# Kernel tuning notes

Hardware: AMD Instinct MI355X
Metric: run time of the kernel (lower is better)

Reference implementation:

```python
import jax, jax.numpy as jnp
import numpy as np
from jax import lax

MASK_STEEP = 4.0
MASK_SHIFT = 0.5
RESIST_TH = 0.225
RESIST_STEEP = 50.0
MAX_DOSE = 1.02
MIN_DOSE = 0.98
KD = 35  # kernel_dim1 == kernel_dim2


def setup_inputs() -> dict:
    key = jax.random.key(0)
    ks = jax.random.split(key, 7)
    N, H, W, K = 2, 1024, 1024, 24
    return {
        "mask_tile": jax.random.uniform(ks[0], (N, 1, H, W), dtype=jnp.float32),
        "kernel_focus_r": jax.random.normal(ks[1], (K, KD, KD), dtype=jnp.float32) * 0.02,
        "kernel_focus_i": jax.random.normal(ks[2], (K, KD, KD), dtype=jnp.float32) * 0.02,
        "kernel_defocus_r": jax.random.normal(ks[3], (K, KD, KD), dtype=jnp.float32) * 0.02,
        "kernel_defocus_i": jax.random.normal(ks[4], (K, KD, KD), dtype=jnp.float32) * 0.02,
        "kernel_focus_scale": jax.random.uniform(ks[5], (K, 1, 1), dtype=jnp.float32),
        "kernel_defocus_scale": jax.random.uniform(ks[6], (K, 1, 1), dtype=jnp.float32),
    }


def _avepool3(x):
    # nn.AvgPool2d(kernel=3, stride=1, pad=1) with count_include_pad=True ==
    # conv with a 3x3 ones/9 kernel and zero padding.
    k = jnp.ones((1, 1, 3, 3), x.dtype) / 9.0
    return lax.conv_general_dilated(
        x, k, window_strides=(1, 1), padding=[(1, 1), (1, 1)],
        dimension_numbers=("NCHW", "OIHW", "NCHW"))


def _dose_branch(spec, dose, kernel, scale, h, w):
    # spec: [N,1,KD,KD] complex; kernel: [K,KD,KD] complex; scale: [K,1,1]
    x = (spec * dose) * kernel[None]                 # [N,K,KD,KD] (repeat_interleave via broadcast, C=1)
    x = jnp.fft.ifft2(x, s=(h, w))                   # zero-pad to full tile, [N,K,h,w] complex
    inten = (x.real * x.real + x.imag * x.imag) * scale[None]
    inten = jnp.sum(inten, axis=1, keepdims=True)    # [N,1,h,w]
    resist = jax.nn.sigmoid(RESIST_STEEP * (inten - RESIST_TH))
    return resist, inten


def reference(mask_tile, kernel_focus_r, kernel_focus_i, kernel_defocus_r,
              kernel_defocus_i, kernel_focus_scale, kernel_defocus_scale):
    n, _, h, w = mask_tile.shape
    off = h // 2 - KD // 2
    mask = _avepool3(mask_tile)
    mask = jax.nn.sigmoid(MASK_STEEP * (mask - MASK_SHIFT))
    mf = jnp.fft.fftshift(jnp.fft.fft2(mask), axes=(-2, -1))  # [N,1,h,w] complex64
    spec = mf[:, :, off:off + KD, off:off + KD]               # [N,1,KD,KD]
    kf = kernel_focus_r + 1j * kernel_focus_i
    kdf = kernel_defocus_r + 1j * kernel_defocus_i
    nominal, x_out = _dose_branch(spec, 1.0, kf, kernel_focus_scale, h, w)
    outer, x_out_max = _dose_branch(spec, MAX_DOSE, kf, kernel_focus_scale, h, w)
    inner, x_out_min = _dose_branch(spec, MIN_DOSE, kdf, kernel_defocus_scale, h, w)
    return (nominal, inner, outer, x_out, x_out_min, x_out_max)
```

## Files before the change

kernel.cpp:

```cpp
#include <hip/hip_runtime.h>
#include <math.h>

#define NBATCH 2
#define HH 1024
#define WW 1024
#define KKER 24
#define KDIM 35
#define NPIX (HH*WW)
#define KSQ (KDIM*KDIM)
#define NDA 69
#define NTAU 9
#define NFR 18
#define VCOLS 43

#define G_OFF 0
#define S_OFF (G_OFF + NBATCH*HH*NFR*2)
#define VP_OFF (S_OFF + NBATCH*KSQ*2)
#define V_OFF (VP_OFF + NBATCH*2*KKER*NDA*KDIM*2)

__device__ __forceinline__ float2 cmadd(float2 p, float2 w, float2 u) {
    return make_float2(fmaf(p.x, w.x, fmaf(-p.y, w.y, u.x)),
                       fmaf(p.x, w.y, fmaf( p.y, w.x, u.y)));
}
__device__ __forceinline__ float sigm(float v) {
    return 1.f / (1.f + expf(-v));
}

__global__ __launch_bounds__(320) void fwd_rows(const float* __restrict__ mt, float* __restrict__ ws) {
    __shared__ __align__(16) float vs[1024];
    __shared__ float row[1056];
    __shared__ float2 twl[1024];
    __shared__ float2 P[16 * NFR];
    int bid = blockIdx.x;
    int n = bid >> 10, y = bid & 1023;
    int t = threadIdx.x;
    const float* base = mt + (size_t)n * NPIX;
    if (t < 256) {
        float4 a = ((const float4*)(base + (size_t)y * WW))[t];
        if (y > 0)    { float4 b = ((const float4*)(base + (size_t)(y - 1) * WW))[t];
                        a.x += b.x; a.y += b.y; a.z += b.z; a.w += b.w; }
        if (y < 1023) { float4 b = ((const float4*)(base + (size_t)(y + 1) * WW))[t];
                        a.x += b.x; a.y += b.y; a.z += b.z; a.w += b.w; }
        ((float4*)vs)[t] = a;
    }
    for (int j = t; j < 1024; j += 320) {
        float s, c;
        sincospif(-2.0f * (float)j * (1.0f / 1024.0f), &s, &c);
        twl[j] = make_float2(c, s);
    }
    __syncthreads();
    for (int x = t; x < 1024; x += 320) {
        float s = vs[x];
        if (x > 0)    s += vs[x - 1];
        if (x < 1023) s += vs[x + 1];
        s *= (1.0f / 9.0f);
        row[x + (x >> 5)] = sigm(4.0f * (s - 0.5f));
    }
    __syncthreads();
    if (t < 16 * NFR) {
        int q = t / NFR, m = t - q * NFR;
        float2 cm = twl[m];
        float ar = 0.f, ai = 0.f;
        #pragma unroll
        for (int sc = 0; sc < 2; ++sc) {
            int xs = q * 64 + sc * 32;
            unsigned j0 = ((unsigned)(m * xs)) & 1023u;
            float2 wv = twl[j0];
            float wr = wv.x, wi = wv.y;
            int rb = xs + (xs >> 5);
            #pragma unroll
            for (int i = 0; i < 32; ++i) {
                float val = row[rb + i];
                ar = fmaf(val, wr, ar);
                ai = fmaf(val, wi, ai);
                float nwr = fmaf(wr, cm.x, -wi * cm.y);
                float nwi = fmaf(wr, cm.y,  wi * cm.x);
                wr = nwr; wi = nwi;
            }
        }
        P[t] = make_float2(ar, ai);
    }
    __syncthreads();
    if (t < NFR) {
        float gr = 0.f, gi = 0.f;
        #pragma unroll
        for (int q = 0; q < 16; ++q) {
            gr += P[q * NFR + t].x;
            gi += P[q * NFR + t].y;
        }
        float2* Gp = (float2*)(ws + G_OFF) + (size_t)(n * HH + y) * NFR + t;
        *Gp = make_float2(gr, gi);
    }
}

__global__ __launch_bounds__(1024) void fwd_cols(float* __restrict__ ws) {
    __shared__ float2 twl[1024];
    __shared__ float2 P[56 * NFR];
    int bid = blockIdx.x;
    int t = threadIdx.x;
    int n = bid / KDIM, a = bid - n * KDIM;
    {
        float s, c;
        sincospif(-2.0f * (float)t * (1.0f / 1024.0f), &s, &c);
        twl[t] = make_float2(c, s);
    }
    __syncthreads();
    if (t < 56 * NFR) {
        int g = t / NFR, mb = t - NFR * g;
        int ys = (g << 10) / 56, ye = ((g + 1) << 10) / 56;
        int ma = a - 17;
        const float2* Gp = (const float2*)(ws + G_OFF) + (size_t)n * HH * NFR + mb;
        float ar = 0.f, ai = 0.f;
        for (int y = ys; y < ye; ++y) {
            float2 g2 = Gp[(size_t)y * NFR];
            float2 cc = twl[((unsigned)(ma * y)) & 1023u];
            ar = fmaf(g2.x, cc.x, ar); ar = fmaf(-g2.y, cc.y, ar);
            ai = fmaf(g2.x, cc.y, ai); ai = fmaf( g2.y, cc.x, ai);
        }
        P[t] = make_float2(ar, ai);
    }
    __syncthreads();
    if (t < NFR) {
        float sr = 0.f, si = 0.f;
        #pragma unroll
        for (int g = 0; g < 56; ++g) { sr += P[g * NFR + t].x; si += P[g * NFR + t].y; }
        float2* Sp = (float2*)(ws + S_OFF) + (size_t)n * KSQ;
        Sp[a * KDIM + (17 + t)] = make_float2(sr, si);
        if (t > 0)
            Sp[(34 - a) * KDIM + (17 - t)] = make_float2(sr, -si);
    }
}

__global__ __launch_bounds__(512) void mk_V(float* __restrict__ ws,
        const float* __restrict__ kfr, const float* __restrict__ kfi,
        const float* __restrict__ kdr, const float* __restrict__ kdi,
        const float* __restrict__ kfs, const float* __restrict__ kds) {
    __shared__ float2 Xp[KDIM * VCOLS];
    __shared__ float2 Vp[9][8][8];
    int bid = blockIdx.x;
    int tau = bid % NTAU; int r = bid / NTAU;
    int k = r % KKER; r /= KKER;
    int br = r & 1; int n = r >> 1;
    int t = threadIdx.x;
    for (int i = t; i < KDIM * VCOLS; i += 512) Xp[i] = make_float2(0.f, 0.f);
    __syncthreads();
    const float* kr = (br ? kdr : kfr) + (size_t)k * KSQ;
    const float* ki = (br ? kdi : kfi) + (size_t)k * KSQ;
    const float* sp = ws + S_OFF + (size_t)n * KSQ * 2;
    for (int i = t; i < KSQ; i += 512) {
        int a = i / KDIM, b = i - a * KDIM;
        float srr = sp[2*i], sii = sp[2*i + 1];
        float krr = kr[i], kii = ki[i];
        Xp[a * VCOLS + b] = make_float2(srr * krr - sii * kii, srr * kii + sii * krr);
    }
    __syncthreads();

    int wv = t >> 6, lane = t & 63;
    int apSlot = lane & 7, dai8 = lane >> 3;
    int dai = tau * 8 + dai8, da = dai - 34;
    int daiHi = tau * 8 + 7; if (daiHi > NDA - 1) daiHi = NDA - 1;
    int apLo = -(daiHi - 34); if (apLo < 0) apLo = 0;
    int apHi = KDIM - (tau * 8 - 34); if (apHi > KDIM) apHi = KDIM;
    bool lv = (dai < NDA);

    int oct = (wv < 3) ? 0 : (wv < 5) ? 1 : (wv < 7) ? 2 : 3;
    int b0w = (wv == 1) ? 12 : (wv == 2) ? 24 : (wv == 4) ? 13 : (wv == 6) ? 9 : 0;
    int b1w = (wv == 0) ? 12 : (wv == 1) ? 24 : (wv == 2) ? 35 :
              (wv == 3) ? 13 : (wv == 4) ? 27 : (wv == 5) ? 9  :
              (wv == 6) ? 19 : 11;
    int npass = (wv == 7) ? 2 : 1;
    for (int p = 0; p < npass; ++p) {
        int db0 = p ? 32 : oct * 8;
        int b0  = p ? 0  : b0w;
        int b1  = p ? 3  : b1w;
        int slot = p ? 8 : wv;
        float2 acc[8];
        #pragma unroll
        for (int j = 0; j < 8; ++j) acc[j] = make_float2(0.f, 0.f);
        for (int ap = apLo + apSlot; ap < apHi; ap += 8) {
            if (lv && ((unsigned)(ap + da) < (unsigned)KDIM)) {
                const float2* rx = Xp + (ap + da) * VCOLS + db0;
                const float2* ry = Xp + ap * VCOLS;
                float2 w[8];
                #pragma unroll
                for (int j = 0; j < 8; ++j) w[j] = rx[b0 + j];
                int bp = b0;
                for (; bp + 8 <= b1; bp += 8) {
                    #pragma unroll
                    for (int u = 0; u < 8; ++u) {
                        float2 yv = ry[bp + u];
                        #pragma unroll
                        for (int j = 0; j < 8; ++j) {
                            acc[j].x = fmaf(w[j].x, yv.x, acc[j].x);
                            acc[j].x = fmaf(w[j].y, yv.y, acc[j].x);
                            acc[j].y = fmaf(w[j].y, yv.x, acc[j].y);
                            acc[j].y = fmaf(-w[j].x, yv.y, acc[j].y);
                        }
                        #pragma unroll
                        for (int j = 0; j < 7; ++j) w[j] = w[j + 1];
                        w[7] = rx[bp + u + 8];
                    }
                }
                for (; bp < b1; ++bp) {
                    float2 yv = ry[bp];
                    #pragma unroll
                    for (int j = 0; j < 8; ++j) {
                        acc[j].x = fmaf(w[j].x, yv.x, acc[j].x);
                        acc[j].x = fmaf(w[j].y, yv.y, acc[j].x);
                        acc[j].y = fmaf(w[j].y, yv.x, acc[j].y);
                        acc[j].y = fmaf(-w[j].x, yv.y, acc[j].y);
                    }
                    #pragma unroll
                    for (int j = 0; j < 7; ++j) w[j] = w[j + 1];
                    w[7] = rx[bp + 8];
                }
            }
        }
        #pragma unroll
        for (int j = 0; j < 8; ++j) {
            acc[j].x += __shfl_xor(acc[j].x, 1); acc[j].y += __shfl_xor(acc[j].y, 1);
            acc[j].x += __shfl_xor(acc[j].x, 2); acc[j].y += __shfl_xor(acc[j].y, 2);
            acc[j].x += __shfl_xor(acc[j].x, 4); acc[j].y += __shfl_xor(acc[j].y, 4);
        }
        if (apSlot == 0) {
            #pragma unroll
            for (int j = 0; j < 8; ++j) Vp[slot][dai8][j] = acc[j];
        }
    }
    __syncthreads();
    if (t < 8 * KDIM) {
        int d8 = t / KDIM, db = t - d8 * KDIM;
        int dai2 = tau * 8 + d8;
        if (dai2 < NDA) {
            int oc = db >> 3, j = db & 7;
            float2 sum;
            if (oc == 0) {
                sum = make_float2(Vp[0][d8][j].x + Vp[1][d8][j].x + Vp[2][d8][j].x,
                                  Vp[0][d8][j].y + Vp[1][d8][j].y + Vp[2][d8][j].y);
            } else if (oc == 1) {
                sum = make_float2(Vp[3][d8][j].x + Vp[4][d8][j].x,
                                  Vp[3][d8][j].y + Vp[4][d8][j].y);
            } else if (oc == 2) {
                sum = make_float2(Vp[5][d8][j].x + Vp[6][d8][j].x,
                                  Vp[5][d8][j].y + Vp[6][d8][j].y);
            } else if (oc == 3) {
                sum = Vp[7][d8][j];
            } else {
                sum = Vp[8][d8][j];
            }
            float s = (br ? kds[k] * (0.98f * 0.98f) : kfs[k]) * 0x1p-40f;
            int nb = n * 2 + br;
            ((float2*)(ws + VP_OFF))[(((size_t)nb * KKER + k) * NDA + dai2) * KDIM + db] =
                make_float2(s * sum.x, s * sum.y);
        }
    }
}

__global__ __launch_bounds__(64) void reduce_V(float* __restrict__ ws) {
    int bid = blockIdx.x;
    int nb = bid / NDA, dai = bid - nb * NDA;
    int t = threadIdx.x;
    if (t < KDIM) {
        const float2* vp = (const float2*)(ws + VP_OFF);
        float sr = 0.f, si = 0.f;
        #pragma unroll
        for (int k = 0; k < KKER; ++k) {
            float2 v = vp[(((size_t)nb * KKER + k) * NDA + dai) * KDIM + t];
            sr += v.x; si += v.y;
        }
        ((float2*)(ws + V_OFF))[((size_t)nb * NDA + dai) * KDIM + t] = make_float2(sr, si);
    }
}

#define YPB 2
__global__ __launch_bounds__(256) void litho_fused(const float* __restrict__ ws,
                                                   float* __restrict__ out) {
    __shared__ float2 twl[1024];
    __shared__ float2 Vl[NDA * KDIM];
    __shared__ float2 Ul[YPB][KDIM];
    int bid = blockIdx.x;
    int yc = bid & 511; int nb = bid >> 9;
    int t = threadIdx.x;
    for (int j = t; j < 1024; j += 256) {
        float s, c;
        sincospif(-2.0f * (float)j * (1.0f / 1024.0f), &s, &c);
        twl[j] = make_float2(c, s);
    }
    const float2* Vg = (const float2*)(ws + V_OFF) + (size_t)nb * NDA * KDIM;
    for (int i = t; i < NDA * KDIM; i += 256) Vl[i] = Vg[i];
    __syncthreads();
    if (t < YPB * KDIM) {
        int yl = t / KDIM, db = t - yl * KDIM;
        int y = yc * YPB + yl;
        float ar = 0.f, ai = 0.f;
        for (int dai = 0; dai < NDA; ++dai) {
            float2 cc = twl[((unsigned)(y * (dai - 34))) & 1023u];
            float cr = cc.x, ci = -cc.y;
            float2 v = Vl[dai * KDIM + db];
            ar = fmaf(v.x, cr, ar); ar = fmaf(-v.y, ci, ar);
            ai = fmaf(v.x, ci, ai); ai = fmaf( v.y, cr, ai);
        }
        Ul[yl][db] = make_float2(ar, ai);
    }
    __syncthreads();
    int n = nb >> 1, br = nb & 1;
    float2 z  = twl[t];              z.y  = -z.y;
    float2 z2 = twl[(2*t) & 1023];   z2.y = -z2.y;
    float2 z3 = twl[(3*t) & 1023];   z3.y = -z3.y;
    float2 w  = twl[(4*t) & 1023];   w.y  = -w.y;
    const size_t OS = (size_t)NBATCH * NPIX;
    #pragma unroll
    for (int yl = 0; yl < YPB; ++yl) {
        int y = yc * YPB + yl;
        float2 P0 = Ul[yl][32], P1 = Ul[yl][33], P2 = Ul[yl][34], P3 = make_float2(0.f, 0.f);
        #pragma unroll
        for (int q = 7; q >= 0; --q) {
            P0 = cmadd(P0, w, Ul[yl][4*q]);
            P1 = cmadd(P1, w, Ul[yl][4*q+1]);
            P2 = cmadd(P2, w, Ul[yl][4*q+2]);
            P3 = cmadd(P3, w, Ul[yl][4*q+3]);
        }
        float U0r = Ul[yl][0].x;
        float A1x = P1.x * z.x  - P1.y * z.y,  A1y = P1.x * z.y  + P1.y * z.x;
        float A2x = P2.x * z2.x - P2.y * z2.y;
        float A3x = P3.x * z3.x - P3.y * z3.y, A3y = P3.x * z3.y + P3.y * z3.x;
        float Re4[4];
        Re4[0] = P0.x + A1x + A2x + A3x;
        Re4[1] = P0.x - A1y - A2x + A3y;
        Re4[2] = P0.x - A1x + A2x - A3x;
        Re4[3] = P0.x + A1y - A2x - A3y;
        size_t obase = (size_t)n * NPIX + (size_t)y * WW;
        if (br == 0) {
            #pragma unroll
            for (int c = 0; c < 4; ++c) {
                int x = t + c * 256;
                float If   = fmaf(2.f, Re4[c], -U0r);
                float Imax = If * (1.02f * 1.02f);
                out[0 * OS + obase + x] = sigm(50.f * (If   - 0.225f));
                out[2 * OS + obase + x] = sigm(50.f * (Imax - 0.225f));
                out[3 * OS + obase + x] = If;
                out[5 * OS + obase + x] = Imax;
            }
        } else {
            #pragma unroll
            for (int c = 0; c < 4; ++c) {
                int x = t + c * 256;
                float Id = fmaf(2.f, Re4[c], -U0r);
                out[1 * OS + obase + x] = sigm(50.f * (Id - 0.225f));
                out[4 * OS + obase + x] = Id;
            }
        }
    }
}

extern "C" void kernel_launch(void* const* d_in, const int* in_sizes, int n_in,
                              void* d_out, int out_size, void* d_ws, size_t ws_size,
                              hipStream_t stream) {
    (void)in_sizes; (void)n_in; (void)out_size; (void)ws_size;
    const float* mt  = (const float*)d_in[0];
    const float* kfr = (const float*)d_in[1];
    const float* kfi = (const float*)d_in[2];
    const float* kdr = (const float*)d_in[3];
    const float* kdi = (const float*)d_in[4];
    const float* kfs = (const float*)d_in[5];
    const float* kds = (const float*)d_in[6];
    float* out = (float*)d_out;
    float* ws  = (float*)d_ws;

    hipLaunchKernelGGL(fwd_rows,    dim3(NBATCH * HH),              dim3(320),  0, stream, mt, ws);
    hipLaunchKernelGGL(fwd_cols,    dim3(NBATCH * KDIM),            dim3(1024), 0, stream, ws);
    hipLaunchKernelGGL(mk_V,        dim3(NBATCH * 2 * KKER * NTAU), dim3(512),  0, stream,
                       ws, kfr, kfi, kdr, kdi, kfs, kds);
    hipLaunchKernelGGL(reduce_V,    dim3(NBATCH * 2 * NDA),         dim3(64),   0, stream, ws);
    hipLaunchKernelGGL(litho_fused, dim3(NBATCH * 2 * 512),         dim3(256),  0, stream, ws, out);
}
```

Before: 154.9 us.

## Fuse column DFT, V build, reduce and output into one persistent kernel

New measurement: 369.7 us. 139% more time.

```diff
diff --git a/kernel.cpp b/kernel.cpp
--- a/kernel.cpp
+++ b/kernel.cpp
@@ -12,11 +12,15 @@
 #define NTAU 9
 #define NFR 18
 #define VCOLS 43
+#define NVBLK (NBATCH*2*KKER*NTAU)
+#define GRID2 1024
+#define COLS_BASE (GRID2 - NBATCH*KDIM)
 
 #define G_OFF 0
 #define S_OFF (G_OFF + NBATCH*HH*NFR*2)
 #define VP_OFF (S_OFF + NBATCH*KSQ*2)
 #define V_OFF (VP_OFF + NBATCH*2*KKER*NDA*KDIM*2)
+#define CNT_OFF (V_OFF + NBATCH*2*NDA*KDIM*2)
 
 __device__ __forceinline__ float2 cmadd(float2 p, float2 w, float2 u) {
     return make_float2(fmaf(p.x, w.x, fmaf(-p.y, w.y, u.x)),
@@ -24,6 +28,13 @@
 }
 __device__ __forceinline__ float sigm(float v) {
     return 1.f / (1.f + expf(-v));
+}
+__device__ __forceinline__ void wait_cnt(int* p, int target) {
+    if (threadIdx.x == 0) {
+        while (atomicAdd(p, 0) < target) __builtin_amdgcn_s_sleep(16);
+    }
+    __syncthreads();
+    __threadfence();
 }
 
 __global__ __launch_bounds__(320) void fwd_rows(const float* __restrict__ mt, float* __restrict__ ws) {
@@ -34,6 +45,7 @@
     int bid = blockIdx.x;
     int n = bid >> 10, y = bid & 1023;
     int t = threadIdx.x;
+    if (bid == 0 && t < 8) ((int*)(ws + CNT_OFF))[t] = 0;
     const float* base = mt + (size_t)n * NPIX;
     if (t < 256) {
         float4 a = ((const float4*)(base + (size_t)y * WW))[t];
@@ -93,102 +105,137 @@
     }
 }
 
-__global__ __launch_bounds__(1024) void fwd_cols(float* __restrict__ ws) {
-    __shared__ float2 twl[1024];
-    __shared__ float2 P[56 * NFR];
-    int bid = blockIdx.x;
-    int t = threadIdx.x;
-    int n = bid / KDIM, a = bid - n * KDIM;
-    {
-        float s, c;
-        sincospif(-2.0f * (float)t * (1.0f / 1024.0f), &s, &c);
-        twl[t] = make_float2(c, s);
-    }
-    __syncthreads();
-    if (t < 56 * NFR) {
-        int g = t / NFR, mb = t - NFR * g;
-        int ys = (g << 10) / 56, ye = ((g + 1) << 10) / 56;
-        int ma = a - 17;
-        const float2* Gp = (const float2*)(ws + G_OFF) + (size_t)n * HH * NFR + mb;
-        float ar = 0.f, ai = 0.f;
-        for (int y = ys; y < ye; ++y) {
-            float2 g2 = Gp[(size_t)y * NFR];
-            float2 cc = twl[((unsigned)(ma * y)) & 1023u];
-            ar = fmaf(g2.x, cc.x, ar); ar = fmaf(-g2.y, cc.y, ar);
-            ai = fmaf(g2.x, cc.y, ai); ai = fmaf( g2.y, cc.x, ai);
-        }
-        P[t] = make_float2(ar, ai);
-    }
-    __syncthreads();
-    if (t < NFR) {
-        float sr = 0.f, si = 0.f;
-        #pragma unroll
-        for (int g = 0; g < 56; ++g) { sr += P[g * NFR + t].x; si += P[g * NFR + t].y; }
-        float2* Sp = (float2*)(ws + S_OFF) + (size_t)n * KSQ;
-        Sp[a * KDIM + (17 + t)] = make_float2(sr, si);
-        if (t > 0)
-            Sp[(34 - a) * KDIM + (17 - t)] = make_float2(sr, -si);
-    }
-}
-
-__global__ __launch_bounds__(512) void mk_V(float* __restrict__ ws,
+__global__ __launch_bounds__(256, 5) void mega2(
         const float* __restrict__ kfr, const float* __restrict__ kfi,
         const float* __restrict__ kdr, const float* __restrict__ kdi,
-        const float* __restrict__ kfs, const float* __restrict__ kds) {
-    __shared__ float2 Xp[KDIM * VCOLS];
-    __shared__ float2 Vp[9][8][8];
-    int bid = blockIdx.x;
-    int tau = bid % NTAU; int r = bid / NTAU;
-    int k = r % KKER; r /= KKER;
-    int br = r & 1; int n = r >> 1;
-    int t = threadIdx.x;
-    for (int i = t; i < KDIM * VCOLS; i += 512) Xp[i] = make_float2(0.f, 0.f);
-    __syncthreads();
-    const float* kr = (br ? kdr : kfr) + (size_t)k * KSQ;
-    const float* ki = (br ? kdi : kfi) + (size_t)k * KSQ;
-    const float* sp = ws + S_OFF + (size_t)n * KSQ * 2;
-    for (int i = t; i < KSQ; i += 512) {
-        int a = i / KDIM, b = i - a * KDIM;
-        float srr = sp[2*i], sii = sp[2*i + 1];
-        float krr = kr[i], kii = ki[i];
-        Xp[a * VCOLS + b] = make_float2(srr * krr - sii * kii, srr * kii + sii * krr);
-    }
-    __syncthreads();
-
-    int wv = t >> 6, lane = t & 63;
-    int apSlot = lane & 7, dai8 = lane >> 3;
-    int dai = tau * 8 + dai8, da = dai - 34;
-    int daiHi = tau * 8 + 7; if (daiHi > NDA - 1) daiHi = NDA - 1;
-    int apLo = -(daiHi - 34); if (apLo < 0) apLo = 0;
-    int apHi = KDIM - (tau * 8 - 34); if (apHi > KDIM) apHi = KDIM;
-    bool lv = (dai < NDA);
-
-    int oct = (wv < 3) ? 0 : (wv < 5) ? 1 : (wv < 7) ? 2 : 3;
-    int b0w = (wv == 1) ? 12 : (wv == 2) ? 24 : (wv == 4) ? 13 : (wv == 6) ? 9 : 0;
-    int b1w = (wv == 0) ? 12 : (wv == 1) ? 24 : (wv == 2) ? 35 :
-              (wv == 3) ? 13 : (wv == 4) ? 27 : (wv == 5) ? 9  :
-              (wv == 6) ? 19 : 11;
-    int npass = (wv == 7) ? 2 : 1;
-    for (int p = 0; p < npass; ++p) {
-        int db0 = p ? 32 : oct * 8;
-        int b0  = p ? 0  : b0w;
-        int b1  = p ? 3  : b1w;
-        int slot = p ? 8 : wv;
-        float2 acc[8];
+        const float* __restrict__ kfs, const float* __restrict__ kds,
+        float* __restrict__ out, float* __restrict__ ws) {
+    __shared__ float2 twl[1024];
+    __shared__ union {
+        struct { float2 P[14 * NFR]; } A;
+        struct { float2 Xp[KDIM * VCOLS]; float2 Vp[9][8][8]; } B;
+        struct { float2 Vl[NDA * KDIM]; float2 Ul[4][KDIM]; } C;
+    } sm;
+    __shared__ int winner;
+    int bid = blockIdx.x, t = threadIdx.x;
+    int* cnt = (int*)(ws + CNT_OFF);
+
+    for (int j = t; j < 1024; j += 256) {
+        float s, c;
+        sincospif(-2.0f * (float)j * (1.0f / 1024.0f), &s, &c);
+        twl[j] = make_float2(c, s);
+    }
+    __syncthreads();
+
+    if (bid >= COLS_BASE) {
+        int cbid = bid - COLS_BASE;
+        int n = cbid / KDIM, a = cbid - n * KDIM;
+        if (t < 14 * NFR) {
+            int g = t / NFR, mb = t - NFR * g;
+            int ys = (g << 10) / 14, ye = ((g + 1) << 10) / 14;
+            int ma = a - 17;
+            const float2* Gp = (const float2*)(ws + G_OFF) + (size_t)n * HH * NFR + mb;
+            float ar = 0.f, ai = 0.f;
+            for (int y = ys; y < ye; ++y) {
+                float2 g2 = Gp[(size_t)y * NFR];
+                float2 cc = twl[((unsigned)(ma * y)) & 1023u];
+                ar = fmaf(g2.x, cc.x, ar); ar = fmaf(-g2.y, cc.y, ar);
+                ai = fmaf(g2.x, cc.y, ai); ai = fmaf( g2.y, cc.x, ai);
+            }
+            sm.A.P[t] = make_float2(ar, ai);
+        }
+        __syncthreads();
+        if (t < NFR) {
+            float sr = 0.f, si = 0.f;
+            #pragma unroll
+            for (int g = 0; g < 14; ++g) { sr += sm.A.P[g * NFR + t].x; si += sm.A.P[g * NFR + t].y; }
+            float2* Sp = (float2*)(ws + S_OFF) + (size_t)n * KSQ;
+            Sp[a * KDIM + (17 + t)] = make_float2(sr, si);
+            if (t > 0)
+                Sp[(34 - a) * KDIM + (17 - t)] = make_float2(sr, -si);
+        }
+        __syncthreads();
+        __threadfence();
+        if (t == 0) atomicAdd(&cnt[n], 1);
+    }
+
+    if (bid < NVBLK) {
+        int tau = bid % NTAU; int r = bid / NTAU;
+        int k = r % KKER; r /= KKER;
+        int br = r & 1; int n = r >> 1;
+        int nb = n * 2 + br;
+        const float* kr = (br ? kdr : kfr) + (size_t)k * KSQ;
+        const float* ki = (br ? kdi : kfi) + (size_t)k * KSQ;
+        float krv[5], kiv[5];
         #pragma unroll
-        for (int j = 0; j < 8; ++j) acc[j] = make_float2(0.f, 0.f);
-        for (int ap = apLo + apSlot; ap < apHi; ap += 8) {
-            if (lv && ((unsigned)(ap + da) < (unsigned)KDIM)) {
-                const float2* rx = Xp + (ap + da) * VCOLS + db0;
-                const float2* ry = Xp + ap * VCOLS;
-                float2 w[8];
-                #pragma unroll
-                for (int j = 0; j < 8; ++j) w[j] = rx[b0 + j];
-                int bp = b0;
-                for (; bp + 8 <= b1; bp += 8) {
+        for (int j = 0; j < 5; ++j) {
+            int i = t + 256 * j;
+            krv[j] = (i < KSQ) ? kr[i] : 0.f;
+            kiv[j] = (i < KSQ) ? ki[i] : 0.f;
+        }
+        float2* Xp = sm.B.Xp;
+        for (int i = t; i < KDIM * 8; i += 256) {
+            int a = i >> 3, c = KDIM + (i & 7);
+            Xp[a * VCOLS + c] = make_float2(0.f, 0.f);
+        }
+        wait_cnt(&cnt[n], KDIM);
+        const float2* spc = (const float2*)(ws + S_OFF) + (size_t)n * KSQ;
+        #pragma unroll
+        for (int j = 0; j < 5; ++j) {
+            int i = t + 256 * j;
+            if (i < KSQ) {
+                int a = i / KDIM, b = i - a * KDIM;
+                float2 s2 = spc[i];
+                Xp[a * VCOLS + b] = make_float2(s2.x * krv[j] - s2.y * kiv[j],
+                                                s2.x * kiv[j] + s2.y * krv[j]);
+            }
+        }
+        __syncthreads();
+
+        int wv = t >> 6, lane = t & 63;
+        int apSlot = lane & 7, dai8 = lane >> 3;
+        int dai = tau * 8 + dai8, da = dai - 34;
+        int daiHi = tau * 8 + 7; if (daiHi > NDA - 1) daiHi = NDA - 1;
+        int apLo = -(daiHi - 34); if (apLo < 0) apLo = 0;
+        int apHi = KDIM - (tau * 8 - 34); if (apHi > KDIM) apHi = KDIM;
+        bool lv = (dai < NDA);
+        int nsp = (wv == 3) ? 3 : 2;
+        for (int ps = 0; ps < nsp; ++ps) {
+            int vs = (ps == 2) ? 8 : wv + 4 * ps;
+            int oct = (vs < 3) ? 0 : (vs < 5) ? 1 : (vs < 7) ? 2 : (vs == 7) ? 3 : 4;
+            int b0 = (vs == 1) ? 12 : (vs == 2) ? 24 : (vs == 4) ? 13 : (vs == 6) ? 9 : 0;
+            int b1 = (vs == 0) ? 12 : (vs == 1) ? 24 : (vs == 2) ? 35 : (vs == 3) ? 13 :
+                     (vs == 4) ? 27 : (vs == 5) ? 9  : (vs == 6) ? 19 : (vs == 7) ? 11 : 3;
+            int db0 = oct * 8;
+            float2 acc[8];
+            #pragma unroll
+            for (int j = 0; j < 8; ++j) acc[j] = make_float2(0.f, 0.f);
+            for (int ap = apLo + apSlot; ap < apHi; ap += 8) {
+                if (lv && ((unsigned)(ap + da) < (unsigned)KDIM)) {
+                    const float2* rx = Xp + (ap + da) * VCOLS + db0;
+                    const float2* ry = Xp + ap * VCOLS;
+                    float2 w[8];
                     #pragma unroll
-                    for (int u = 0; u < 8; ++u) {
-                        float2 yv = ry[bp + u];
+                    for (int j = 0; j < 8; ++j) w[j] = rx[b0 + j];
+                    int bp = b0;
+                    for (; bp + 8 <= b1; bp += 8) {
+                        #pragma unroll
+                        for (int u = 0; u < 8; ++u) {
+                            float2 yv = ry[bp + u];
+                            #pragma unroll
+                            for (int j = 0; j < 8; ++j) {
+                                acc[j].x = fmaf(w[j].x, yv.x, acc[j].x);
+                                acc[j].x = fmaf(w[j].y, yv.y, acc[j].x);
+                                acc[j].y = fmaf(w[j].y, yv.x, acc[j].y);
+                                acc[j].y = fmaf(-w[j].x, yv.y, acc[j].y);
+                            }
+                            #pragma unroll
+                            for (int j = 0; j < 7; ++j) w[j] = w[j + 1];
+                            w[7] = rx[bp + u + 8];
+                        }
+                    }
+                    for (; bp < b1; ++bp) {
+                        float2 yv = ry[bp];
                         #pragma unroll
                         for (int j = 0; j < 8; ++j) {
                             acc[j].x = fmaf(w[j].x, yv.x, acc[j].x);
@@ -198,156 +245,139 @@
                         }
                         #pragma unroll
                         for (int j = 0; j < 7; ++j) w[j] = w[j + 1];
-                        w[7] = rx[bp + u + 8];
+                        w[7] = rx[bp + 8];
                     }
                 }
-                for (; bp < b1; ++bp) {
-                    float2 yv = ry[bp];
-                    #pragma unroll
-                    for (int j = 0; j < 8; ++j) {
-                        acc[j].x = fmaf(w[j].x, yv.x, acc[j].x);
-                        acc[j].x = fmaf(w[j].y, yv.y, acc[j].x);
-                        acc[j].y = fmaf(w[j].y, yv.x, acc[j].y);
-                        acc[j].y = fmaf(-w[j].x, yv.y, acc[j].y);
-                    }
-                    #pragma unroll
-                    for (int j = 0; j < 7; ++j) w[j] = w[j + 1];
-                    w[7] = rx[bp + 8];
+            }
+            #pragma unroll
+            for (int j = 0; j < 8; ++j) {
+                acc[j].x += __shfl_xor(acc[j].x, 1); acc[j].y += __shfl_xor(acc[j].y, 1);
+                acc[j].x += __shfl_xor(acc[j].x, 2); acc[j].y += __shfl_xor(acc[j].y, 2);
+                acc[j].x += __shfl_xor(acc[j].x, 4); acc[j].y += __shfl_xor(acc[j].y, 4);
+            }
+            if (apSlot == 0) {
+                #pragma unroll
+                for (int j = 0; j < 8; ++j) sm.B.Vp[vs][dai8][j] = acc[j];
+            }
+        }
+        __syncthreads();
+        if (t < 8 * KDIM) {
+            int d8 = t / KDIM, db = t - d8 * KDIM;
+            int dai2 = tau * 8 + d8;
+            if (dai2 < NDA) {
+                int oc = db >> 3, j = db & 7;
+                float2 sum;
+                if (oc == 0) {
+                    sum = make_float2(sm.B.Vp[0][d8][j].x + sm.B.Vp[1][d8][j].x + sm.B.Vp[2][d8][j].x,
+                                      sm.B.Vp[0][d8][j].y + sm.B.Vp[1][d8][j].y + sm.B.Vp[2][d8][j].y);
+                } else if (oc == 1) {
+                    sum = make_float2(sm.B.Vp[3][d8][j].x + sm.B.Vp[4][d8][j].x,
+                                      sm.B.Vp[3][d8][j].y + sm.B.Vp[4][d8][j].y);
+                } else if (oc == 2) {
+                    sum = make_float2(sm.B.Vp[5][d8][j].x + sm.B.Vp[6][d8][j].x,
+                                      sm.B.Vp[5][d8][j].y + sm.B.Vp[6][d8][j].y);
+                } else if (oc == 3) {
+                    sum = sm.B.Vp[7][d8][j];
+                } else {
+                    sum = sm.B.Vp[8][d8][j];
                 }
-            }
-        }
+                float s = (br ? kds[k] * (0.98f * 0.98f) : kfs[k]) * 0x1p-40f;
+                ((float2*)(ws + VP_OFF))[(((size_t)nb * KKER + k) * NDA + dai2) * KDIM + db] =
+                    make_float2(s * sum.x, s * sum.y);
+            }
+        }
+        __syncthreads();
+        __threadfence();
+        if (t == 0) winner = (atomicAdd(&cnt[2 + nb], 1) == NVBLK / 4 - 1);
+        __syncthreads();
+        if (winner) {
+            __threadfence();
+            const float2* vp = (const float2*)(ws + VP_OFF) + (size_t)nb * KKER * NDA * KDIM;
+            float2* vo = (float2*)(ws + V_OFF) + (size_t)nb * NDA * KDIM;
+            for (int i = t; i < NDA * KDIM; i += 256) {
+                float sr = 0.f, si = 0.f;
+                #pragma unroll
+                for (int kk = 0; kk < KKER; ++kk) {
+                    float2 v = vp[(size_t)kk * NDA * KDIM + i];
+                    sr += v.x; si += v.y;
+                }
+                vo[i] = make_float2(sr, si);
+            }
+            __syncthreads();
+            __threadfence();
+            if (t == 0) atomicAdd(&cnt[6], 1);
+        }
+    }
+
+    wait_cnt(&cnt[6], 4);
+    __syncthreads();
+    {
+        int nb = bid >> 8, yc = bid & 255;
+        int y0 = yc * 4;
+        const float2* Vg = (const float2*)(ws + V_OFF) + (size_t)nb * NDA * KDIM;
+        for (int i = t; i < NDA * KDIM; i += 256) sm.C.Vl[i] = Vg[i];
+        __syncthreads();
+        if (t < 4 * KDIM) {
+            int yl = t / KDIM, db = t - KDIM * yl;
+            int y = y0 + yl;
+            float ar = 0.f, ai = 0.f;
+            for (int dai = 0; dai < NDA; ++dai) {
+                float2 cc = twl[((unsigned)(y * (dai - 34))) & 1023u];
+                float cr = cc.x, ci = -cc.y;
+                float2 v = sm.C.Vl[dai * KDIM + db];
+                ar = fmaf(v.x, cr, ar); ar = fmaf(-v.y, ci, ar);
+                ai = fmaf(v.x, ci, ai); ai = fmaf( v.y, cr, ai);
+            }
+            sm.C.Ul[yl][db] = make_float2(ar, ai);
+        }
+        __syncthreads();
+        int n = nb >> 1, br = nb & 1;
+        float2 z  = twl[t];              z.y  = -z.y;
+        float2 z2 = twl[(2*t) & 1023];   z2.y = -z2.y;
+        float2 z3 = twl[(3*t) & 1023];   z3.y = -z3.y;
+        float2 w  = twl[(4*t) & 1023];   w.y  = -w.y;
+        const size_t OS = (size_t)NBATCH * NPIX;
         #pragma unroll
-        for (int j = 0; j < 8; ++j) {
-            acc[j].x += __shfl_xor(acc[j].x, 1); acc[j].y += __shfl_xor(acc[j].y, 1);
-            acc[j].x += __shfl_xor(acc[j].x, 2); acc[j].y += __shfl_xor(acc[j].y, 2);
-            acc[j].x += __shfl_xor(acc[j].x, 4); acc[j].y += __shfl_xor(acc[j].y, 4);
-        }
-        if (apSlot == 0) {
+        for (int yl = 0; yl < 4; ++yl) {
+            int y = y0 + yl;
+            float2 P0 = sm.C.Ul[yl][32], P1 = sm.C.Ul[yl][33];
+            float2 P2 = sm.C.Ul[yl][34], P3 = make_float2(0.f, 0.f);
             #pragma unroll
-            for (int j = 0; j < 8; ++j) Vp[slot][dai8][j] = acc[j];
-        }
-    }
-    __syncthreads();
-    if (t < 8 * KDIM) {
-        int d8 = t / KDIM, db = t - d8 * KDIM;
-        int dai2 = tau * 8 + d8;
-        if (dai2 < NDA) {
-            int oc = db >> 3, j = db & 7;
-            float2 sum;
-            if (oc == 0) {
-                sum = make_float2(Vp[0][d8][j].x + Vp[1][d8][j].x + Vp[2][d8][j].x,
-                                  Vp[0][d8][j].y + Vp[1][d8][j].y + Vp[2][d8][j].y);
-            } else if (oc == 1) {
-                sum = make_float2(Vp[3][d8][j].x + Vp[4][d8][j].x,
-                                  Vp[3][d8][j].y + Vp[4][d8][j].y);
-            } else if (oc == 2) {
-                sum = make_float2(Vp[5][d8][j].x + Vp[6][d8][j].x,
-                                  Vp[5][d8][j].y + Vp[6][d8][j].y);
-            } else if (oc == 3) {
-                sum = Vp[7][d8][j];
+            for (int q = 7; q >= 0; --q) {
+                P0 = cmadd(P0, w, sm.C.Ul[yl][4*q]);
+                P1 = cmadd(P1, w, sm.C.Ul[yl][4*q+1]);
+                P2 = cmadd(P2, w, sm.C.Ul[yl][4*q+2]);
+                P3 = cmadd(P3, w, sm.C.Ul[yl][4*q+3]);
+            }
+            float U0r = sm.C.Ul[yl][0].x;
+            float A1x = P1.x * z.x  - P1.y * z.y,  A1y = P1.x * z.y  + P1.y * z.x;
+            float A2x = P2.x * z2.x - P2.y * z2.y;
+            float A3x = P3.x * z3.x - P3.y * z3.y, A3y = P3.x * z3.y + P3.y * z3.x;
+            float Re4[4];
+            Re4[0] = P0.x + A1x + A2x + A3x;
+            Re4[1] = P0.x - A1y - A2x + A3y;
+            Re4[2] = P0.x - A1x + A2x - A3x;
+            Re4[3] = P0.x + A1y - A2x - A3y;
+            size_t obase = (size_t)n * NPIX + (size_t)y * WW;
+            if (br == 0) {
+                #pragma unroll
+                for (int c = 0; c < 4; ++c) {
+                    int x = t + c * 256;
+                    float If   = fmaf(2.f, Re4[c], -U0r);
+                    float Imax = If * (1.02f * 1.02f);
+                    out[0 * OS + obase + x] = sigm(50.f * (If   - 0.225f));
+                    out[2 * OS + obase + x] = sigm(50.f * (Imax - 0.225f));
+                    out[3 * OS + obase + x] = If;
+                    out[5 * OS + obase + x] = Imax;
+                }
             } else {
-                sum = Vp[8][d8][j];
-            }
-            float s = (br ? kds[k] * (0.98f * 0.98f) : kfs[k]) * 0x1p-40f;
-            int nb = n * 2 + br;
-            ((float2*)(ws + VP_OFF))[(((size_t)nb * KKER + k) * NDA + dai2) * KDIM + db] =
-                make_float2(s * sum.x, s * sum.y);
-        }
-    }
-}
-
-__global__ __launch_bounds__(64) void reduce_V(float* __restrict__ ws) {
-    int bid = blockIdx.x;
-    int nb = bid / NDA, dai = bid - nb * NDA;
-    int t = threadIdx.x;
-    if (t < KDIM) {
-        const float2* vp = (const float2*)(ws + VP_OFF);
-        float sr = 0.f, si = 0.f;
-        #pragma unroll
-        for (int k = 0; k < KKER; ++k) {
-            float2 v = vp[(((size_t)nb * KKER + k) * NDA + dai) * KDIM + t];
-            sr += v.x; si += v.y;
-        }
-        ((float2*)(ws + V_OFF))[((size_t)nb * NDA + dai) * KDIM + t] = make_float2(sr, si);
-    }
-}
-
-#define YPB 2
-__global__ __launch_bounds__(256) void litho_fused(const float* __restrict__ ws,
-                                                   float* __restrict__ out) {
-    __shared__ float2 twl[1024];
-    __shared__ float2 Vl[NDA * KDIM];
-    __shared__ float2 Ul[YPB][KDIM];
-    int bid = blockIdx.x;
-    int yc = bid & 511; int nb = bid >> 9;
-    int t = threadIdx.x;
-    for (int j = t; j < 1024; j += 256) {
-        float s, c;
-        sincospif(-2.0f * (float)j * (1.0f / 1024.0f), &s, &c);
-        twl[j] = make_float2(c, s);
-    }
-    const float2* Vg = (const float2*)(ws + V_OFF) + (size_t)nb * NDA * KDIM;
-    for (int i = t; i < NDA * KDIM; i += 256) Vl[i] = Vg[i];
-    __syncthreads();
-    if (t < YPB * KDIM) {
-        int yl = t / KDIM, db = t - yl * KDIM;
-        int y = yc * YPB + yl;
-        float ar = 0.f, ai = 0.f;
-        for (int dai = 0; dai < NDA; ++dai) {
-            float2 cc = twl[((unsigned)(y * (dai - 34))) & 1023u];
-            float cr = cc.x, ci = -cc.y;
-            float2 v = Vl[dai * KDIM + db];
-            ar = fmaf(v.x, cr, ar); ar = fmaf(-v.y, ci, ar);
-            ai = fmaf(v.x, ci, ai); ai = fmaf( v.y, cr, ai);
-        }
-        Ul[yl][db] = make_float2(ar, ai);
-    }
-    __syncthreads();
-    int n = nb >> 1, br = nb & 1;
-    float2 z  = twl[t];              z.y  = -z.y;
-    float2 z2 = twl[(2*t) & 1023];   z2.y = -z2.y;
-    float2 z3 = twl[(3*t) & 1023];   z3.y = -z3.y;
-    float2 w  = twl[(4*t) & 1023];   w.y  = -w.y;
-    const size_t OS = (size_t)NBATCH * NPIX;
-    #pragma unroll
-    for (int yl = 0; yl < YPB; ++yl) {
-        int y = yc * YPB + yl;
-        float2 P0 = Ul[yl][32], P1 = Ul[yl][33], P2 = Ul[yl][34], P3 = make_float2(0.f, 0.f);
-        #pragma unroll
-        for (int q = 7; q >= 0; --q) {
-            P0 = cmadd(P0, w, Ul[yl][4*q]);
-            P1 = cmadd(P1, w, Ul[yl][4*q+1]);
-            P2 = cmadd(P2, w, Ul[yl][4*q+2]);
-            P3 = cmadd(P3, w, Ul[yl][4*q+3]);
-        }
-        float U0r = Ul[yl][0].x;
-        float A1x = P1.x * z.x  - P1.y * z.y,  A1y = P1.x * z.y  + P1.y * z.x;
-        float A2x = P2.x * z2.x - P2.y * z2.y;
-        float A3x = P3.x * z3.x - P3.y * z3.y, A3y = P3.x * z3.y + P3.y * z3.x;
-        float Re4[4];
-        Re4[0] = P0.x + A1x + A2x + A3x;
-        Re4[1] = P0.x - A1y - A2x + A3y;
-        Re4[2] = P0.x - A1x + A2x - A3x;
-        Re4[3] = P0.x + A1y - A2x - A3y;
-        size_t obase = (size_t)n * NPIX + (size_t)y * WW;
-        if (br == 0) {
-            #pragma unroll
-            for (int c = 0; c < 4; ++c) {
-                int x = t + c * 256;
-                float If   = fmaf(2.f, Re4[c], -U0r);
-                float Imax = If * (1.02f * 1.02f);
-                out[0 * OS + obase + x] = sigm(50.f * (If   - 0.225f));
-                out[2 * OS + obase + x] = sigm(50.f * (Imax - 0.225f));
-                out[3 * OS + obase + x] = If;
-                out[5 * OS + obase + x] = Imax;
-            }
-        } else {
-            #pragma unroll
-            for (int c = 0; c < 4; ++c) {
-                int x = t + c * 256;
-                float Id = fmaf(2.f, Re4[c], -U0r);
-                out[1 * OS + obase + x] = sigm(50.f * (Id - 0.225f));
-                out[4 * OS + obase + x] = Id;
+                #pragma unroll
+                for (int c = 0; c < 4; ++c) {
+                    int x = t + c * 256;
+                    float Id = fmaf(2.f, Re4[c], -U0r);
+                    out[1 * OS + obase + x] = sigm(50.f * (Id - 0.225f));
+                    out[4 * OS + obase + x] = Id;
+                }
             }
         }
     }
@@ -367,10 +397,7 @@
     float* out = (float*)d_out;
     float* ws  = (float*)d_ws;
 
-    hipLaunchKernelGGL(fwd_rows,    dim3(NBATCH * HH),              dim3(320),  0, stream, mt, ws);
-    hipLaunchKernelGGL(fwd_cols,    dim3(NBATCH * KDIM),            dim3(1024), 0, stream, ws);
-    hipLaunchKernelGGL(mk_V,        dim3(NBATCH * 2 * KKER * NTAU), dim3(512),  0, stream,
-                       ws, kfr, kfi, kdr, kdi, kfs, kds);
-    hipLaunchKernelGGL(reduce_V,    dim3(NBATCH * 2 * NDA),         dim3(64),   0, stream, ws);
-    hipLaunchKernelGGL(litho_fused, dim3(NBATCH * 2 * 512),         dim3(256),  0, stream, ws, out);
-}
+    hipLaunchKernelGGL(fwd_rows, dim3(NBATCH * HH), dim3(320), 0, stream, mt, ws);
+    hipLaunchKernelGGL(mega2,    dim3(GRID2),       dim3(256), 0, stream,
+                       kfr, kfi, kdr, kdi, kfs, kds, out, ws);
+}
```

## Fold kernel-sum reduction into mk_V and litho_fused, drop reduce_V

Applied to the files above, without the earlier changes.

After: 165.4 us. 1.07x slower.

```diff
diff --git a/kernel.cpp b/kernel.cpp
--- a/kernel.cpp
+++ b/kernel.cpp
@@ -12,11 +12,11 @@
 #define NTAU 9
 #define NFR 18
 #define VCOLS 43
+#define KC 8
 
 #define G_OFF 0
 #define S_OFF (G_OFF + NBATCH*HH*NFR*2)
 #define VP_OFF (S_OFF + NBATCH*KSQ*2)
-#define V_OFF (VP_OFF + NBATCH*2*KKER*NDA*KDIM*2)
 
 __device__ __forceinline__ float2 cmadd(float2 p, float2 w, float2 u) {
     return make_float2(fmaf(p.x, w.x, fmaf(-p.y, w.y, u.x)),
@@ -139,21 +139,15 @@
     __shared__ float2 Vp[9][8][8];
     int bid = blockIdx.x;
     int tau = bid % NTAU; int r = bid / NTAU;
-    int k = r % KKER; r /= KKER;
+    int kg = r % KC; r /= KC;
     int br = r & 1; int n = r >> 1;
     int t = threadIdx.x;
-    for (int i = t; i < KDIM * VCOLS; i += 512) Xp[i] = make_float2(0.f, 0.f);
-    __syncthreads();
-    const float* kr = (br ? kdr : kfr) + (size_t)k * KSQ;
-    const float* ki = (br ? kdi : kfi) + (size_t)k * KSQ;
-    const float* sp = ws + S_OFF + (size_t)n * KSQ * 2;
-    for (int i = t; i < KSQ; i += 512) {
-        int a = i / KDIM, b = i - a * KDIM;
-        float srr = sp[2*i], sii = sp[2*i + 1];
-        float krr = kr[i], kii = ki[i];
-        Xp[a * VCOLS + b] = make_float2(srr * krr - sii * kii, srr * kii + sii * krr);
-    }
-    __syncthreads();
+    for (int i = t; i < 9 * 64; i += 512) ((float2*)Vp)[i] = make_float2(0.f, 0.f);
+    for (int i = t; i < KDIM * 8; i += 512) {
+        int a = i >> 3, c = KDIM + (i & 7);
+        Xp[a * VCOLS + c] = make_float2(0.f, 0.f);
+    }
+    const float* spb = ws + S_OFF + (size_t)n * KSQ * 2;
 
     int wv = t >> 6, lane = t & 63;
     int apSlot = lane & 7, dai8 = lane >> 3;
@@ -162,33 +156,60 @@
     int apLo = -(daiHi - 34); if (apLo < 0) apLo = 0;
     int apHi = KDIM - (tau * 8 - 34); if (apHi > KDIM) apHi = KDIM;
     bool lv = (dai < NDA);
-
     int oct = (wv < 3) ? 0 : (wv < 5) ? 1 : (wv < 7) ? 2 : 3;
     int b0w = (wv == 1) ? 12 : (wv == 2) ? 24 : (wv == 4) ? 13 : (wv == 6) ? 9 : 0;
     int b1w = (wv == 0) ? 12 : (wv == 1) ? 24 : (wv == 2) ? 35 :
               (wv == 3) ? 13 : (wv == 4) ? 27 : (wv == 5) ? 9  :
               (wv == 6) ? 19 : 11;
     int npass = (wv == 7) ? 2 : 1;
-    for (int p = 0; p < npass; ++p) {
-        int db0 = p ? 32 : oct * 8;
-        int b0  = p ? 0  : b0w;
-        int b1  = p ? 3  : b1w;
-        int slot = p ? 8 : wv;
-        float2 acc[8];
-        #pragma unroll
-        for (int j = 0; j < 8; ++j) acc[j] = make_float2(0.f, 0.f);
-        for (int ap = apLo + apSlot; ap < apHi; ap += 8) {
-            if (lv && ((unsigned)(ap + da) < (unsigned)KDIM)) {
-                const float2* rx = Xp + (ap + da) * VCOLS + db0;
-                const float2* ry = Xp + ap * VCOLS;
-                float2 w[8];
-                #pragma unroll
-                for (int j = 0; j < 8; ++j) w[j] = rx[b0 + j];
-                int bp = b0;
-                for (; bp + 8 <= b1; bp += 8) {
+
+    for (int kk = 0; kk < 3; ++kk) {
+        int k = kg * 3 + kk;
+        const float* kr = (br ? kdr : kfr) + (size_t)k * KSQ;
+        const float* ki = (br ? kdi : kfi) + (size_t)k * KSQ;
+        __syncthreads();
+        for (int i = t; i < KSQ; i += 512) {
+            int a = i / KDIM, b = i - a * KDIM;
+            float srr = spb[2*i], sii = spb[2*i + 1];
+            float krr = kr[i], kii = ki[i];
+            Xp[a * VCOLS + b] = make_float2(srr * krr - sii * kii, srr * kii + sii * krr);
+        }
+        __syncthreads();
+        float s = (br ? kds[k] * (0.98f * 0.98f) : kfs[k]) * 0x1p-40f;
+        for (int p = 0; p < npass; ++p) {
+            int db0 = p ? 32 : oct * 8;
+            int b0  = p ? 0  : b0w;
+            int b1  = p ? 3  : b1w;
+            int slot = p ? 8 : wv;
+            float2 acc[8];
+            #pragma unroll
+            for (int j = 0; j < 8; ++j) acc[j] = make_float2(0.f, 0.f);
+            for (int ap = apLo + apSlot; ap < apHi; ap += 8) {
+                if (lv && ((unsigned)(ap + da) < (unsigned)KDIM)) {
+                    const float2* rx = Xp + (ap + da) * VCOLS + db0;
+                    const float2* ry = Xp + ap * VCOLS;
+                    float2 w[8];
                     #pragma unroll
-                    for (int u = 0; u < 8; ++u) {
-                        float2 yv = ry[bp + u];
+                    for (int j = 0; j < 8; ++j) w[j] = rx[b0 + j];
+                    int bp = b0;
+                    for (; bp + 8 <= b1; bp += 8) {
+                        #pragma unroll
+                        for (int u = 0; u < 8; ++u) {
+                            float2 yv = ry[bp + u];
+                            #pragma unroll
+                            for (int j = 0; j < 8; ++j) {
+                                acc[j].x = fmaf(w[j].x, yv.x, acc[j].x);
+                                acc[j].x = fmaf(w[j].y, yv.y, acc[j].x);
+                                acc[j].y = fmaf(w[j].y, yv.x, acc[j].y);
+                                acc[j].y = fmaf(-w[j].x, yv.y, acc[j].y);
+                            }
+                            #pragma unroll
+                            for (int j = 0; j < 7; ++j) w[j] = w[j + 1];
+                            w[7] = rx[bp + u + 8];
+                        }
+                    }
+                    for (; bp < b1; ++bp) {
+                        float2 yv = ry[bp];
                         #pragma unroll
                         for (int j = 0; j < 8; ++j) {
                             acc[j].x = fmaf(w[j].x, yv.x, acc[j].x);
@@ -198,33 +219,24 @@
                         }
                         #pragma unroll
                         for (int j = 0; j < 7; ++j) w[j] = w[j + 1];
-                        w[7] = rx[bp + u + 8];
+                        w[7] = rx[bp + 8];
                     }
                 }
-                for (; bp < b1; ++bp) {
-                    float2 yv = ry[bp];
-                    #pragma unroll
-                    for (int j = 0; j < 8; ++j) {
-                        acc[j].x = fmaf(w[j].x, yv.x, acc[j].x);
-                        acc[j].x = fmaf(w[j].y, yv.y, acc[j].x);
-                        acc[j].y = fmaf(w[j].y, yv.x, acc[j].y);
-                        acc[j].y = fmaf(-w[j].x, yv.y, acc[j].y);
-                    }
-                    #pragma unroll
-                    for (int j = 0; j < 7; ++j) w[j] = w[j + 1];
-                    w[7] = rx[bp + 8];
+            }
+            #pragma unroll
+            for (int j = 0; j < 8; ++j) {
+                acc[j].x += __shfl_xor(acc[j].x, 1); acc[j].y += __shfl_xor(acc[j].y, 1);
+                acc[j].x += __shfl_xor(acc[j].x, 2); acc[j].y += __shfl_xor(acc[j].y, 2);
+                acc[j].x += __shfl_xor(acc[j].x, 4); acc[j].y += __shfl_xor(acc[j].y, 4);
+            }
+            if (apSlot == 0) {
+                #pragma unroll
+                for (int j = 0; j < 8; ++j) {
+                    float2 v = Vp[slot][dai8][j];
+                    Vp[slot][dai8][j] = make_float2(fmaf(s, acc[j].x, v.x),
+                                                    fmaf(s, acc[j].y, v.y));
                 }
             }
-        }
-        #pragma unroll
-        for (int j = 0; j < 8; ++j) {
-            acc[j].x += __shfl_xor(acc[j].x, 1); acc[j].y += __shfl_xor(acc[j].y, 1);
-            acc[j].x += __shfl_xor(acc[j].x, 2); acc[j].y += __shfl_xor(acc[j].y, 2);
-            acc[j].x += __shfl_xor(acc[j].x, 4); acc[j].y += __shfl_xor(acc[j].y, 4);
-        }
-        if (apSlot == 0) {
-            #pragma unroll
-            for (int j = 0; j < 8; ++j) Vp[slot][dai8][j] = acc[j];
         }
     }
     __syncthreads();
@@ -248,50 +260,41 @@
             } else {
                 sum = Vp[8][d8][j];
             }
-            float s = (br ? kds[k] * (0.98f * 0.98f) : kfs[k]) * 0x1p-40f;
             int nb = n * 2 + br;
-            ((float2*)(ws + VP_OFF))[(((size_t)nb * KKER + k) * NDA + dai2) * KDIM + db] =
-                make_float2(s * sum.x, s * sum.y);
-        }
-    }
-}
-
-__global__ __launch_bounds__(64) void reduce_V(float* __restrict__ ws) {
-    int bid = blockIdx.x;
-    int nb = bid / NDA, dai = bid - nb * NDA;
-    int t = threadIdx.x;
-    if (t < KDIM) {
-        const float2* vp = (const float2*)(ws + VP_OFF);
-        float sr = 0.f, si = 0.f;
-        #pragma unroll
-        for (int k = 0; k < KKER; ++k) {
-            float2 v = vp[(((size_t)nb * KKER + k) * NDA + dai) * KDIM + t];
-            sr += v.x; si += v.y;
-        }
-        ((float2*)(ws + V_OFF))[((size_t)nb * NDA + dai) * KDIM + t] = make_float2(sr, si);
-    }
-}
-
-#define YPB 2
+            ((float2*)(ws + VP_OFF))[(((size_t)nb * KC + kg) * NDA + dai2) * KDIM + db] = sum;
+        }
+    }
+}
+
+#define YPB 4
 __global__ __launch_bounds__(256) void litho_fused(const float* __restrict__ ws,
                                                    float* __restrict__ out) {
     __shared__ float2 twl[1024];
     __shared__ float2 Vl[NDA * KDIM];
     __shared__ float2 Ul[YPB][KDIM];
     int bid = blockIdx.x;
-    int yc = bid & 511; int nb = bid >> 9;
+    int yc = bid & 255; int nb = bid >> 8;
+    int y0 = yc * YPB;
     int t = threadIdx.x;
     for (int j = t; j < 1024; j += 256) {
         float s, c;
         sincospif(-2.0f * (float)j * (1.0f / 1024.0f), &s, &c);
         twl[j] = make_float2(c, s);
     }
-    const float2* Vg = (const float2*)(ws + V_OFF) + (size_t)nb * NDA * KDIM;
-    for (int i = t; i < NDA * KDIM; i += 256) Vl[i] = Vg[i];
-    __syncthreads();
-    if (t < YPB * KDIM) {
-        int yl = t / KDIM, db = t - yl * KDIM;
-        int y = yc * YPB + yl;
+    const float2* Vg = (const float2*)(ws + VP_OFF) + (size_t)nb * KC * NDA * KDIM;
+    for (int i = t; i < NDA * KDIM; i += 256) {
+        float sr = 0.f, si = 0.f;
+        #pragma unroll
+        for (int g = 0; g < KC; ++g) {
+            float2 v = Vg[(size_t)g * NDA * KDIM + i];
+            sr += v.x; si += v.y;
+        }
+        Vl[i] = make_float2(sr, si);
+    }
+    __syncthreads();
+    for (int task = t; task < YPB * KDIM; task += 256) {
+        int yl = task / KDIM, db = task - KDIM * yl;
+        int y = y0 + yl;
         float ar = 0.f, ai = 0.f;
         for (int dai = 0; dai < NDA; ++dai) {
             float2 cc = twl[((unsigned)(y * (dai - 34))) & 1023u];
@@ -311,7 +314,7 @@
     const size_t OS = (size_t)NBATCH * NPIX;
     #pragma unroll
     for (int yl = 0; yl < YPB; ++yl) {
-        int y = yc * YPB + yl;
+        int y = y0 + yl;
         float2 P0 = Ul[yl][32], P1 = Ul[yl][33], P2 = Ul[yl][34], P3 = make_float2(0.f, 0.f);
         #pragma unroll
         for (int q = 7; q >= 0; --q) {
@@ -367,10 +370,9 @@
     float* out = (float*)d_out;
     float* ws  = (float*)d_ws;
 
-    hipLaunchKernelGGL(fwd_rows,    dim3(NBATCH * HH),              dim3(320),  0, stream, mt, ws);
-    hipLaunchKernelGGL(fwd_cols,    dim3(NBATCH * KDIM),            dim3(1024), 0, stream, ws);
-    hipLaunchKernelGGL(mk_V,        dim3(NBATCH * 2 * KKER * NTAU), dim3(512),  0, stream,
+    hipLaunchKernelGGL(fwd_rows,    dim3(NBATCH * HH),          dim3(320),  0, stream, mt, ws);
+    hipLaunchKernelGGL(fwd_cols,    dim3(NBATCH * KDIM),        dim3(1024), 0, stream, ws);
+    hipLaunchKernelGGL(mk_V,        dim3(NBATCH * 2 * KC * NTAU), dim3(512), 0, stream,
                        ws, kfr, kfi, kdr, kdi, kfs, kds);
-    hipLaunchKernelGGL(reduce_V,    dim3(NBATCH * 2 * NDA),         dim3(64),   0, stream, ws);
-    hipLaunchKernelGGL(litho_fused, dim3(NBATCH * 2 * 512),         dim3(256),  0, stream, ws, out);
-}
+    hipLaunchKernelGGL(litho_fused, dim3(NBATCH * 2 * 256),     dim3(256),  0, stream, ws, out);
+}
```
